# Kernel optimization log

Hardware: AMD Instinct MI355X
Metric: run time of the kernel (lower is better)

## Reference

```python
import jax, jax.numpy as jnp
import numpy as np

IN_FEATURES = 4096
OUT_FEATURES = 4096
RANK = 16
ALPHA = 32.0
SCALING = ALPHA / RANK


def setup_inputs() -> dict:
    key = jax.random.key(0)
    k_x, k_a, k_b = jax.random.split(key, 3)
    x = jax.random.normal(k_x, (4, 2048, IN_FEATURES), dtype=jnp.float32)
    # kaiming-uniform(a=sqrt(5)) for A: bound = sqrt(6/((1+5)*fan_in)) = 1/sqrt(fan_in)
    bound = 1.0 / np.sqrt(IN_FEATURES)
    lora_A = jax.random.uniform(k_a, (RANK, IN_FEATURES), dtype=jnp.float32,
                                minval=-bound, maxval=bound)
    # B is zero-init in the module; use small random values so gradients are non-trivial
    lora_B = jax.random.normal(k_b, (OUT_FEATURES, RANK), dtype=jnp.float32) * 0.01
    return {"x": x, "lora_A": lora_A, "lora_B": lora_B}


def reference(x, lora_A, lora_B):
    # dropout=0 -> identity. F.linear(x, B@A) == x @ A^T @ B^T; keep low-rank order.
    h = jnp.einsum('bsd,rd->bsr', x, lora_A)      # [B,S,rank]
    out = jnp.einsum('bsr,or->bso', h, lora_B)    # [B,S,out_features]
    return out * SCALING
```

## Files before the change

kernel.cpp:

```cpp
#include <hip/hip_runtime.h>


#define IN_F  4096
#define OUT_F 4096
#define RANK  16

__global__ __launch_bounds__(256) void k_transpose(const float* __restrict__ A,
                                                   float* __restrict__ At) {
    int idx = blockIdx.x * 256 + threadIdx.x;
    int r = idx >> 12;
    int k = idx & 4095;
    At[k * RANK + r] = A[idx];
}

__global__ __launch_bounds__(256) void k_stage1(const float* __restrict__ x,
                                                const float* __restrict__ At,
                                                float* __restrict__ hp) {
    __shared__ float xs[4 * 64 * 36];
    const int tid  = threadIdx.x;
    const int w    = __builtin_amdgcn_readfirstlane(tid >> 6);
    const int lane = tid & 63;
    const int b    = blockIdx.x;
    const int row0 = (b >> 2) * 64;
    const int kw   = (b & 3) * 1024 + w * 256;

    float p[RANK];
#pragma unroll
    for (int i = 0; i < RANK; ++i) p[i] = 0.0f;

    float* xw = xs + w * (64 * 36);
    const int rs = lane >> 3;
    const int kl = (lane & 7) * 4;

    for (int c = 0; c < 8; ++c) {
        const int kc = kw + c * 32;
#pragma unroll
        for (int i = 0; i < 8; ++i) {
            const int r = i * 8 + rs;
            const float4 v = *(const float4*)(x + (size_t)(row0 + r) * IN_F + (kc + kl));
            *(float4*)(xw + r * 36 + kl) = v;
        }
        for (int k = 0; k < 32; k += 4) {
            const float4 xv = *(const float4*)(xw + lane * 36 + k);
            const float* a  = At + (size_t)(kc + k) * RANK;
#pragma unroll
            for (int r = 0; r < RANK; ++r) p[r] += xv.x * a[r];
#pragma unroll
            for (int r = 0; r < RANK; ++r) p[r] += xv.y * a[RANK + r];
#pragma unroll
            for (int r = 0; r < RANK; ++r) p[r] += xv.z * a[2 * RANK + r];
#pragma unroll
            for (int r = 0; r < RANK; ++r) p[r] += xv.w * a[3 * RANK + r];
        }
    }
    const int ks = (b & 3) * 4 + w;
    const size_t row = (size_t)row0 + lane;
#pragma unroll
    for (int r = 0; r < RANK; ++r)
        hp[(row * RANK + r) * 16 + ks] = p[r];
}

__global__ __launch_bounds__(256) void k_stage2(const float* __restrict__ hp,
                                                const float* __restrict__ B,
                                                float* __restrict__ out) {
    __shared__ float hs[64 * RANK];
    const int tid  = threadIdx.x;
    const int b    = blockIdx.x;
    const int row0 = (b >> 2) * 64;
    const int o    = (b & 3) * 1024 + tid * 4;

#pragma unroll
    for (int i = 0; i < 4; ++i) {
        const int idx = i * 256 + tid;
        const float4* h4 = (const float4*)(hp + ((size_t)row0 * RANK + idx) * 16);
        const float4 a = h4[0], c = h4[1], d = h4[2], e = h4[3];
        hs[idx] = 2.0f * (a.x + a.y + a.z + a.w + c.x + c.y + c.z + c.w +
                          d.x + d.y + d.z + d.w + e.x + e.y + e.z + e.w);
    }

    float4 breg[16];
    const float4* B4 = (const float4*)B;
#pragma unroll
    for (int i = 0; i < 16; ++i) breg[i] = B4[(size_t)o * 4 + i];
    const float* bf = (const float*)breg;
    __syncthreads();

    for (int r = 0; r < 64; ++r) {
        const float4 h0 = *(const float4*)(hs + r * RANK);
        const float4 h1 = *(const float4*)(hs + r * RANK + 4);
        const float4 h2 = *(const float4*)(hs + r * RANK + 8);
        const float4 h3 = *(const float4*)(hs + r * RANK + 12);
        const float hv[16] = {h0.x, h0.y, h0.z, h0.w, h1.x, h1.y, h1.z, h1.w,
                              h2.x, h2.y, h2.z, h2.w, h3.x, h3.y, h3.z, h3.w};
        float4 acc = {0.f, 0.f, 0.f, 0.f};
#pragma unroll
        for (int rho = 0; rho < 16; ++rho) {
            acc.x += hv[rho] * bf[0 * 16 + rho];
            acc.y += hv[rho] * bf[1 * 16 + rho];
            acc.z += hv[rho] * bf[2 * 16 + rho];
            acc.w += hv[rho] * bf[3 * 16 + rho];
        }
        *(float4*)(out + (size_t)(row0 + r) * OUT_F + o) = acc;
    }
}

extern "C" void kernel_launch(void* const* d_in, const int* in_sizes, int n_in,
                              void* d_out, int out_size, void* d_ws, size_t ws_size,
                              hipStream_t stream) {
    const float* x  = (const float*)d_in[0];
    const float* A  = (const float*)d_in[1];
    const float* Bm = (const float*)d_in[2];
    float* out = (float*)d_out;
    float* At  = (float*)d_ws;
    float* hp  = (float*)((char*)d_ws + (size_t)IN_F * RANK * 4);

    k_transpose<<<256, 256, 0, stream>>>(A, At);
    k_stage1<<<512, 256, 0, stream>>>(x, At, hp);
    k_stage2<<<512, 256, 0, stream>>>(hp, Bm, out);
}
```

Baseline: 294.2 us.

## Split stage1 K dimension 32 ways, drop LDS staging, halve stage2 row tile

Stage1 now gives each wavefront a 64-row by 128-column K slice, with 32 K-splits in total. Each lane reads its own row straight from global memory as float4 loads, replacing the shared-memory staging, and the grid doubles to 1024 blocks. Partial results are written in a ks-major layout as contiguous float4s. Stage2 reduces the 32 partials per element, which means more global reads, and processes 32 rows per block over 1024 blocks. The aim is more parallelism and occupancy in the x-streaming stage. The cost is per-lane strided row access (each lane touches a different 16KB-strided row), which may hurt coalescing, plus a larger partial buffer.

```diff
diff --git a/kernel.cpp b/kernel.cpp
--- a/kernel.cpp
+++ b/kernel.cpp
@@ -4,6 +4,8 @@
 #define IN_F  4096
 #define OUT_F 4096
 #define RANK  16
+#define KSPLIT 32
+#define KSLICE 128
 
 __global__ __launch_bounds__(256) void k_transpose(const float* __restrict__ A,
                                                    float* __restrict__ At) {
@@ -16,76 +18,77 @@
 __global__ __launch_bounds__(256) void k_stage1(const float* __restrict__ x,
                                                 const float* __restrict__ At,
                                                 float* __restrict__ hp) {
-    __shared__ float xs[4 * 64 * 36];
     const int tid  = threadIdx.x;
     const int w    = __builtin_amdgcn_readfirstlane(tid >> 6);
     const int lane = tid & 63;
-    const int b    = blockIdx.x;
-    const int row0 = (b >> 2) * 64;
-    const int kw   = (b & 3) * 1024 + w * 256;
+    const int g    = blockIdx.x * 4 + w;
+    const int rg   = g >> 5;
+    const int ks   = g & (KSPLIT - 1);
+    const size_t row = (size_t)rg * 64 + lane;
+    const int k0   = ks * KSLICE;
+
+    const float* xr = x + row * IN_F + k0;
 
     float p[RANK];
 #pragma unroll
-    for (int i = 0; i < RANK; ++i) p[i] = 0.0f;
+    for (int r = 0; r < RANK; ++r) p[r] = 0.0f;
 
-    float* xw = xs + w * (64 * 36);
-    const int rs = lane >> 3;
-    const int kl = (lane & 7) * 4;
-
+#pragma unroll 2
     for (int c = 0; c < 8; ++c) {
-        const int kc = kw + c * 32;
+        float4 v[4];
 #pragma unroll
-        for (int i = 0; i < 8; ++i) {
-            const int r = i * 8 + rs;
-            const float4 v = *(const float4*)(x + (size_t)(row0 + r) * IN_F + (kc + kl));
-            *(float4*)(xw + r * 36 + kl) = v;
-        }
-        for (int k = 0; k < 32; k += 4) {
-            const float4 xv = *(const float4*)(xw + lane * 36 + k);
-            const float* a  = At + (size_t)(kc + k) * RANK;
+        for (int q = 0; q < 4; ++q)
+            v[q] = *(const float4*)(xr + c * 16 + q * 4);
+        const float* a = At + (size_t)(k0 + c * 16) * RANK;
 #pragma unroll
-            for (int r = 0; r < RANK; ++r) p[r] += xv.x * a[r];
+        for (int q = 0; q < 4; ++q) {
+            const float* aq = a + q * 64;
 #pragma unroll
-            for (int r = 0; r < RANK; ++r) p[r] += xv.y * a[RANK + r];
+            for (int r = 0; r < RANK; ++r) p[r] += v[q].x * aq[r];
 #pragma unroll
-            for (int r = 0; r < RANK; ++r) p[r] += xv.z * a[2 * RANK + r];
+            for (int r = 0; r < RANK; ++r) p[r] += v[q].y * aq[RANK + r];
 #pragma unroll
-            for (int r = 0; r < RANK; ++r) p[r] += xv.w * a[3 * RANK + r];
+            for (int r = 0; r < RANK; ++r) p[r] += v[q].z * aq[2 * RANK + r];
+#pragma unroll
+            for (int r = 0; r < RANK; ++r) p[r] += v[q].w * aq[3 * RANK + r];
         }
     }
-    const int ks = (b & 3) * 4 + w;
-    const size_t row = (size_t)row0 + lane;
-#pragma unroll
-    for (int r = 0; r < RANK; ++r)
-        hp[(row * RANK + r) * 16 + ks] = p[r];
+
+    float4* o = (float4*)(hp + ((size_t)ks * 8192 + row) * RANK);
+    o[0] = make_float4(p[0],  p[1],  p[2],  p[3]);
+    o[1] = make_float4(p[4],  p[5],  p[6],  p[7]);
+    o[2] = make_float4(p[8],  p[9],  p[10], p[11]);
+    o[3] = make_float4(p[12], p[13], p[14], p[15]);
 }
 
 __global__ __launch_bounds__(256) void k_stage2(const float* __restrict__ hp,
                                                 const float* __restrict__ B,
                                                 float* __restrict__ out) {
-    __shared__ float hs[64 * RANK];
+    __shared__ float hs[32 * RANK];
     const int tid  = threadIdx.x;
     const int b    = blockIdx.x;
-    const int row0 = (b >> 2) * 64;
-    const int o    = (b & 3) * 1024 + tid * 4;
+    const int row0 = (b >> 2) * 32;
+    const int col  = (b & 3) * 1024 + tid * 4;
 
 #pragma unroll
-    for (int i = 0; i < 4; ++i) {
+    for (int i = 0; i < 2; ++i) {
         const int idx = i * 256 + tid;
-        const float4* h4 = (const float4*)(hp + ((size_t)row0 * RANK + idx) * 16);
-        const float4 a = h4[0], c = h4[1], d = h4[2], e = h4[3];
-        hs[idx] = 2.0f * (a.x + a.y + a.z + a.w + c.x + c.y + c.z + c.w +
-                          d.x + d.y + d.z + d.w + e.x + e.y + e.z + e.w);
+        const float* src = hp + (size_t)row0 * RANK + idx;
+        float s = 0.0f;
+#pragma unroll
+        for (int ks = 0; ks < KSPLIT; ++ks)
+            s += src[(size_t)ks * 8192 * RANK];
+        hs[idx] = 2.0f * s;
     }
 
     float4 breg[16];
-    const float4* B4 = (const float4*)B;
+    const float4* B4 = (const float4*)(B + (size_t)col * RANK);
 #pragma unroll
-    for (int i = 0; i < 16; ++i) breg[i] = B4[(size_t)o * 4 + i];
+    for (int i = 0; i < 16; ++i) breg[i] = B4[i];
     const float* bf = (const float*)breg;
     __syncthreads();
 
-    for (int r = 0; r < 64; ++r) {
+    for (int r = 0; r < 32; ++r) {
         const float4 h0 = *(const float4*)(hs + r * RANK);
         const float4 h1 = *(const float4*)(hs + r * RANK + 4);
         const float4 h2 = *(const float4*)(hs + r * RANK + 8);
@@ -94,13 +97,13 @@
                               h2.x, h2.y, h2.z, h2.w, h3.x, h3.y, h3.z, h3.w};
         float4 acc = {0.f, 0.f, 0.f, 0.f};
 #pragma unroll
-        for (int rho = 0; rho < 16; ++rho) {
-            acc.x += hv[rho] * bf[0 * 16 + rho];
-            acc.y += hv[rho] * bf[1 * 16 + rho];
-            acc.z += hv[rho] * bf[2 * 16 + rho];
-            acc.w += hv[rho] * bf[3 * 16 + rho];
+        for (int rho = 0; rho < RANK; ++rho) {
+            acc.x += hv[rho] * bf[0 * RANK + rho];
+            acc.y += hv[rho] * bf[1 * RANK + rho];
+            acc.z += hv[rho] * bf[2 * RANK + rho];
+            acc.w += hv[rho] * bf[3 * RANK + rho];
         }
-        *(float4*)(out + (size_t)(row0 + r) * OUT_F + o) = acc;
+        *(float4*)(out + (size_t)(row0 + r) * OUT_F + col) = acc;
     }
 }
 
@@ -115,6 +118,6 @@
     float* hp  = (float*)((char*)d_ws + (size_t)IN_F * RANK * 4);
 
     k_transpose<<<256, 256, 0, stream>>>(A, At);
-    k_stage1<<<512, 256, 0, stream>>>(x, At, hp);
-    k_stage2<<<512, 256, 0, stream>>>(hp, Bm, out);
+    k_stage1<<<1024, 256, 0, stream>>>(x, At, hp);
+    k_stage2<<<1024, 256, 0, stream>>>(hp, Bm, out);
 }
```

After: 291.2 us. Within noise of the previous version (-1.0%).
